# Kernel tuning notes

Measured on AMD Instinct MI355X. Metric: run time of the kernel, lower is better.

The kernel has to match this reference:

```python
import jax, jax.numpy as jnp
import numpy as np

N, DEG, D, L = 20000, 32, 128, 2
EPS = 1e-7
MAX_TANH_ARG = 1.0 - 1e-5


def _logmap0(x, sqrt_c):
    # Poincare ball log map at the origin: artanh(sqrt(c)||x||) * x / (sqrt(c)||x||)
    norm = jnp.maximum(jnp.linalg.norm(x, axis=-1, keepdims=True), EPS)
    arg = jnp.minimum(sqrt_c * norm, MAX_TANH_ARG)
    return jnp.arctanh(arg) * x / (sqrt_c * norm)


def _expmap0(v, sqrt_c):
    # Poincare ball exp map at the origin: tanh(sqrt(c)||v||) * v / (sqrt(c)||v||)
    norm = jnp.maximum(jnp.linalg.norm(v, axis=-1, keepdims=True), EPS)
    return jnp.tanh(sqrt_c * norm) * v / (sqrt_c * norm)


def setup_inputs() -> dict:
    key = jax.random.key(0)
    ks = jax.random.split(key, 7)
    neighbors = jax.random.randint(ks[0], (N, DEG), 0, N)  # fixed in-degree predecessor lists
    node_embeddings = jax.random.normal(ks[1], (N, D), dtype=jnp.float32)
    in_proj_w = jax.random.normal(ks[2], (L, 3 * D, D), dtype=jnp.float32) * 0.02
    in_proj_b = jax.random.normal(ks[3], (L, 3 * D), dtype=jnp.float32) * 0.02
    out_proj_w = jax.random.normal(ks[4], (L, D, D), dtype=jnp.float32) * 0.02
    out_proj_b = jax.random.normal(ks[5], (L, D), dtype=jnp.float32) * 0.02
    curvature = jnp.array([-1.0], dtype=jnp.float32)
    return {
        'neighbors': neighbors,
        'node_embeddings': node_embeddings,
        'curvature': curvature,
        'in_proj_w': in_proj_w,
        'in_proj_b': in_proj_b,
        'out_proj_w': out_proj_w,
        'out_proj_b': out_proj_b,
    }


def reference(neighbors, node_embeddings, curvature, in_proj_w, in_proj_b, out_proj_w, out_proj_b):
    sqrt_c = jnp.sqrt(jnp.abs(curvature[0]))
    scale = 1.0 / np.sqrt(D)  # torch MHA scales q by 1/sqrt(head_dim)
    x = node_embeddings
    for l in range(L):
        t = _logmap0(x, sqrt_c)                       # [N, d] tangent features
        Wq, Wk, Wv = in_proj_w[l, :D], in_proj_w[l, D:2 * D], in_proj_w[l, 2 * D:]
        bq, bk, bv = in_proj_b[l, :D], in_proj_b[l, D:2 * D], in_proj_b[l, 2 * D:]
        q = t @ Wq.T + bq                             # [N, d]
        k = t @ Wk.T + bk
        v = t @ Wv.T + bv
        kn = k[neighbors]                             # [N, deg, d] gather over predecessors
        vn = v[neighbors]                             # [N, deg, d]
        scores = jnp.einsum('nd,nkd->nk', q, kn) * scale
        attn = jax.nn.softmax(scores, axis=-1)        # [N, deg]
        h = jnp.einsum('nk,nkd->nd', attn, vn)        # [N, d]
        h = h @ out_proj_w[l].T + out_proj_b[l]
        x = _expmap0(h, sqrt_c)
    return x
```

## Files before the change

kernel.cpp:

```cpp
#include <hip/hip_runtime.h>

#define N_NODES 20000
#define N_PAD   20032
#define DEG 32
#define D 128
#define EPS 1e-7f
#define MAX_TANH_ARG (1.0f - 1e-5f)
#define SCORE_SCALE 0.08838834764831845f
#define MTILES 313

typedef short bf16x8 __attribute__((ext_vector_type(8)));
typedef float f32x4 __attribute__((ext_vector_type(4)));
typedef float f32x2 __attribute__((ext_vector_type(2)));

__device__ __forceinline__ float b2f(unsigned short u) {
  union { unsigned int i; float f; } x; x.i = ((unsigned int)u) << 16; return x.f;
}
__device__ __forceinline__ unsigned short f2b(float f) {
  union { float f; unsigned int i; } x; x.f = f;
  unsigned int r = x.i + 0x7FFFu + ((x.i >> 16) & 1u);
  return (unsigned short)(r >> 16);
}
__device__ __forceinline__ bool inputs_are_bf16(const void* curv) {
  return *(const unsigned short*)curv != 0;
}
__device__ __forceinline__ float read_sqrt_c(const void* c) {
  unsigned short u = *(const unsigned short*)c;
  float cv = (u == 0) ? *(const float*)c : b2f(u);
  return sqrtf(fabsf(cv));
}
__device__ __forceinline__ float atanh_fast(float x) {
  return 0.5f * __logf((1.f + x) / (1.f - x));
}
__device__ __forceinline__ float tanh_over_y(float y) {
  float e = __expf(-2.f * y);
  return (1.f - e) / ((1.f + e) * y);
}
__device__ __forceinline__ float load1(const void* p, size_t off, bool bf) {
  return bf ? b2f(((const unsigned short*)p)[off]) : ((const float*)p)[off];
}

__device__ __forceinline__ unsigned char f2fp8(float v) {
#if __has_builtin(__builtin_amdgcn_cvt_pk_fp8_f32)
  int p = __builtin_amdgcn_cvt_pk_fp8_f32(v, 0.f, 0, false);
  return (unsigned char)(p & 0xFF);
#else
  union { float f; unsigned u; } x; x.f = v;
  unsigned s = (x.u >> 31) << 7;
  float a = fminf(fabsf(v), 448.f);
  int q = (int)rintf(a * 512.f);
  if (q < 8) return (unsigned char)(s | q);
  int e; float m = frexpf(a, &e);
  int E = e - 1 + 7;
  int mi = (int)rintf(m * 16.f) - 8;
  if (mi == 8) { mi = 0; E += 1; }
  if (E > 15) { E = 15; mi = 6; }
  if (E < 1)  { return (unsigned char)(s | ((int)rintf(a * 512.f) & 7)); }
  return (unsigned char)(s | (E << 3) | mi);
#endif
}
__device__ __forceinline__ void fp8x8_decode_sw(uint2 w, float* f) {
#pragma unroll
  for (int i = 0; i < 8; i++) {
    unsigned char u = (i < 4) ? (unsigned char)(w.x >> (8 * i))
                              : (unsigned char)(w.y >> (8 * (i - 4)));
    int e = (u >> 3) & 15, m = u & 7;
    float mag = e ? ldexpf((float)(8 + m), e - 10) : ldexpf((float)m, -9);
    f[i] = (u & 0x80) ? -mag : mag;
  }
}
__device__ __forceinline__ void fp8x8_decode2(uint2 w, f32x2* f) {
#if __has_builtin(__builtin_amdgcn_cvt_pk_f32_fp8)
  f[0] = __builtin_amdgcn_cvt_pk_f32_fp8((int)w.x, false);
  f[1] = __builtin_amdgcn_cvt_pk_f32_fp8((int)w.x, true);
  f[2] = __builtin_amdgcn_cvt_pk_f32_fp8((int)w.y, false);
  f[3] = __builtin_amdgcn_cvt_pk_f32_fp8((int)w.y, true);
#else
  float t[8];
  fp8x8_decode_sw(w, t);
  f[0] = {t[0], t[1]}; f[1] = {t[2], t[3]};
  f[2] = {t[4], t[5]}; f[3] = {t[6], t[7]};
#endif
}

template <int NT>
__device__ __forceinline__ void stage_W(const void* W, size_t woff, bool srcbf,
                                        unsigned short* W_lds, int tid) {
  if (srcbf) {
#pragma unroll
    for (int c = 0; c < 16384 / (NT * 8); c++) {
      int idx = c * NT * 8 + tid * 8;
      bf16x8 v = *(const bf16x8*)((const unsigned short*)W + woff + idx);
      int row = idx >> 7, col = idx & 127;
      *(bf16x8*)&W_lds[row * 136 + col] = v;
    }
  } else {
#pragma unroll
    for (int c = 0; c < 16384 / (NT * 4); c++) {
      int idx = c * NT * 4 + tid * 4;
      float4 v = *(const float4*)((const float*)W + woff + idx);
      int row = idx >> 7, col = idx & 127;
      unsigned short* p = &W_lds[row * 136 + col];
      p[0] = f2b(v.x); p[1] = f2b(v.y); p[2] = f2b(v.z); p[3] = f2b(v.w);
    }
  }
}

__device__ __forceinline__ void qkv_from_lds(
    const bf16x8* a, const unsigned short* W_lds,
    const void* bias, size_t boff, bool srcbf,
    int m0, int quad, int l16,
    unsigned short* qout, unsigned char* out8, bool isq) {
#pragma unroll
  for (int half = 0; half < 2; half++) {
#pragma unroll
    for (int s = 0; s < 4; s++) {
      int n = half * 64 + s * 16 + l16;
      f32x4 c = {0.f, 0.f, 0.f, 0.f};
#pragma unroll
      for (int kk = 0; kk < 4; kk++) {
        bf16x8 bfv = *(const bf16x8*)&W_lds[n * 136 + quad * 8 + kk * 32];
        c = __builtin_amdgcn_mfma_f32_16x16x32_bf16(a[kk], bfv, c, 0, 0, 0);
      }
      float bv = load1(bias, boff + n, srcbf);
#pragma unroll
      for (int r = 0; r < 4; r++) {
        int m = m0 + quad * 4 + r;
        float val = c[r] + bv;
        if (isq) qout[(size_t)m * D + n] = f2b(val);
        else     out8[(size_t)m * D + n] = f2fp8(val);
      }
    }
  }
}

__device__ __forceinline__ void outproj_acc_frag(
    const bf16x8* a, const unsigned short* W_lds,
    int quad, int l16, f32x4* acc) {
#pragma unroll
  for (int s = 0; s < 8; s++) {
    f32x4 c = {0.f, 0.f, 0.f, 0.f};
#pragma unroll
    for (int kk = 0; kk < 4; kk++) {
      bf16x8 bfv = *(const bf16x8*)&W_lds[(s * 16 + l16) * 136 + quad * 8 + kk * 32];
      c = __builtin_amdgcn_mfma_f32_16x16x32_bf16(a[kk], bfv, c, 0, 0, 0);
    }
    acc[s] = c;
  }
}

__global__ __launch_bounds__(256) void lqkv_kernel(
    const void* __restrict__ xin,
    const void* __restrict__ in_w, const void* __restrict__ in_b,
    unsigned short* __restrict__ qout,
    unsigned char* __restrict__ kout, unsigned char* __restrict__ vout,
    const void* __restrict__ curv) {
  __shared__ unsigned short t_lds[64 * 136];
  __shared__ unsigned short W_lds[128 * 136];
  int tid = threadIdx.x;
  int lane = tid & 63;
  int wave = tid >> 6;
  int mbase = blockIdx.x * 64;
  int y = blockIdx.y;
  bool srcbf = inputs_are_bf16(curv);
  float sqc = read_sqrt_c(curv);

  stage_W<256>(in_w, (size_t)y * 128 * D, srcbf, W_lds, tid);

  {
    int rl = tid >> 3;
    int c8 = tid & 7;
#pragma unroll
    for (int pass = 0; pass < 2; pass++) {
      int r = pass * 32 + rl;
      int m = mbase + r;
      float xv[16];
      if (m < N_NODES) {
        if (srcbf) {
          const bf16x8* xp = (const bf16x8*)((const unsigned short*)xin + (size_t)m * D + c8 * 16);
          bf16x8 u0 = xp[0], u1 = xp[1];
#pragma unroll
          for (int i = 0; i < 8; i++) { xv[i] = b2f((unsigned short)u0[i]); xv[8 + i] = b2f((unsigned short)u1[i]); }
        } else {
          const float4* xp = (const float4*)((const float*)xin + (size_t)m * D + c8 * 16);
#pragma unroll
          for (int i = 0; i < 4; i++) {
            float4 v = xp[i];
            xv[i * 4 + 0] = v.x; xv[i * 4 + 1] = v.y; xv[i * 4 + 2] = v.z; xv[i * 4 + 3] = v.w;
          }
        }
      } else {
#pragma unroll
        for (int i = 0; i < 16; i++) xv[i] = 0.f;
      }
      float ss = 0.f;
#pragma unroll
      for (int i = 0; i < 16; i++) ss += xv[i] * xv[i];
      ss += __shfl_xor(ss, 1); ss += __shfl_xor(ss, 2); ss += __shfl_xor(ss, 4);
      float norm = fmaxf(sqrtf(ss), EPS);
      float arg  = fminf(sqc * norm, MAX_TANH_ARG);
      float sfac = atanh_fast(arg) / (sqc * norm);
      bf16x8 o0, o1;
#pragma unroll
      for (int i = 0; i < 8; i++) {
        o0[i] = (short)f2b(xv[i] * sfac);
        o1[i] = (short)f2b(xv[8 + i] * sfac);
      }
      *(bf16x8*)&t_lds[r * 136 + c8 * 16]     = o0;
      *(bf16x8*)&t_lds[r * 136 + c8 * 16 + 8] = o1;
    }
  }
  __syncthreads();

  int quad = lane >> 4, l16 = lane & 15;
  bf16x8 a[4];
#pragma unroll
  for (int kk = 0; kk < 4; kk++)
    a[kk] = *(const bf16x8*)&t_lds[(wave * 16 + l16) * 136 + quad * 8 + kk * 32];

  qkv_from_lds(a, W_lds, in_b, (size_t)y * 128, srcbf,
               mbase + wave * 16, quad, l16,
               qout, (y == 1) ? kout : vout, y == 0);
}

__global__ __launch_bounds__(256) void attn_kernel(
    const int* __restrict__ nbrs,
    const unsigned short* __restrict__ qb,
    const unsigned char* __restrict__ k8,
    const unsigned char* __restrict__ v8,
    unsigned short* __restrict__ hout) {
  int gid  = blockIdx.x * 256 + threadIdx.x;
  int node = gid >> 6;
  int lane = gid & 63;
  if (node >= N_NODES) return;
  int g = lane >> 4;
  int s = lane & 15;

  f32x2 qr2[4];
  {
    bf16x8 qv = *(const bf16x8*)(qb + (size_t)node * D + s * 8);
#pragma unroll
    for (int i = 0; i < 4; i++) {
      qr2[i][0] = b2f((unsigned short)qv[2 * i]);
      qr2[i][1] = b2f((unsigned short)qv[2 * i + 1]);
    }
  }
  int idx[8];
#pragma unroll
  for (int jj = 0; jj < 8; jj++) idx[jj] = nbrs[node * DEG + jj * 4 + g];

  uint2 kreg[8], vreg[8];
#pragma unroll
  for (int jj = 0; jj < 8; jj++)
    kreg[jj] = *(const uint2*)(k8 + (size_t)idx[jj] * D + s * 8);
#pragma unroll
  for (int jj = 0; jj < 8; jj++)
    vreg[jj] = *(const uint2*)(v8 + (size_t)idx[jj] * D + s * 8);

  float sc[8];
#pragma unroll
  for (int jj = 0; jj < 8; jj++) {
    f32x2 kf[4];
    fp8x8_decode2(kreg[jj], kf);
    f32x2 acc2 = kf[0] * qr2[0];
    acc2 += kf[1] * qr2[1];
    acc2 += kf[2] * qr2[2];
    acc2 += kf[3] * qr2[3];
    float p = acc2[0] + acc2[1];
    p += __shfl_xor(p, 1); p += __shfl_xor(p, 2);
    p += __shfl_xor(p, 4); p += __shfl_xor(p, 8);
    sc[jj] = p * SCORE_SCALE;
  }
  float mx = sc[0];
#pragma unroll
  for (int jj = 1; jj < 8; jj++) mx = fmaxf(mx, sc[jj]);
  mx = fmaxf(mx, __shfl_xor(mx, 16));
  mx = fmaxf(mx, __shfl_xor(mx, 32));
  float sum = 0.f;
#pragma unroll
  for (int jj = 0; jj < 8; jj++) { sc[jj] = __expf(sc[jj] - mx); sum += sc[jj]; }
  sum += __shfl_xor(sum, 16);
  sum += __shfl_xor(sum, 32);
  float inv = 1.f / sum;

  f32x2 hv2[4];
#pragma unroll
  for (int i = 0; i < 4; i++) hv2[i] = {0.f, 0.f};
#pragma unroll
  for (int jj = 0; jj < 8; jj++) {
    float aw = sc[jj] * inv;
    f32x2 aw2 = {aw, aw};
    f32x2 vf[4];
    fp8x8_decode2(vreg[jj], vf);
#pragma unroll
    for (int i = 0; i < 4; i++) hv2[i] += aw2 * vf[i];
  }
  float hv[8];
#pragma unroll
  for (int i = 0; i < 4; i++) { hv[2 * i] = hv2[i][0]; hv[2 * i + 1] = hv2[i][1]; }
#pragma unroll
  for (int i = 0; i < 8; i++) {
    hv[i] += __shfl_xor(hv[i], 16);
    hv[i] += __shfl_xor(hv[i], 32);
  }
  if (g == 0) {
    bf16x8 o;
#pragma unroll
    for (int i = 0; i < 8; i++) o[i] = (short)f2b(hv[i]);
    *(bf16x8*)(hout + (size_t)node * D + s * 8) = o;
  }
}

__global__ __launch_bounds__(256) void op_qkv_kernel(
    const unsigned short* __restrict__ h,
    const void* __restrict__ out_w, const void* __restrict__ out_b,
    const void* __restrict__ in_w, const void* __restrict__ in_b,
    unsigned short* __restrict__ qout,
    unsigned char* __restrict__ kout, unsigned char* __restrict__ vout,
    const void* __restrict__ curv) {
  __shared__ unsigned short t_lds[64 * 136];
  __shared__ unsigned short W_lds[128 * 136];
  int tid = threadIdx.x;
  int lane = tid & 63;
  int wave = tid >> 6;
  int quad = lane >> 4, l16 = lane & 15;
  int m0 = blockIdx.x * 64 + wave * 16;
  int y = blockIdx.y;
  bool srcbf = inputs_are_bf16(curv);

  stage_W<256>(out_w, 0, srcbf, W_lds, tid);
  __syncthreads();
  {
    bf16x8 a[4];
    const short* arow = (const short*)h + (size_t)(m0 + l16) * D + quad * 8;
#pragma unroll
    for (int kk = 0; kk < 4; kk++) a[kk] = *(const bf16x8*)(arow + kk * 32);
    f32x4 acc[8];
    outproj_acc_frag(a, W_lds, quad, l16, acc);
#pragma unroll
    for (int s = 0; s < 8; s++) {
      float bv = load1(out_b, s * 16 + l16, srcbf);
#pragma unroll
      for (int r = 0; r < 4; r++) {
        int rloc = wave * 16 + quad * 4 + r;
        t_lds[rloc * 136 + s * 16 + l16] = f2b(acc[s][r] + bv);
      }
    }
  }
  __syncthreads();

  bf16x8 a[4];
#pragma unroll
  for (int kk = 0; kk < 4; kk++)
    a[kk] = *(const bf16x8*)&t_lds[(wave * 16 + l16) * 136 + quad * 8 + kk * 32];
  stage_W<256>(in_w, (size_t)384 * D + (size_t)y * 128 * D, srcbf, W_lds, tid);
  __syncthreads();

  qkv_from_lds(a, W_lds, in_b, (size_t)384 + y * 128, srcbf,
               m0, quad, l16, qout, (y == 1) ? kout : vout, y == 0);
}

__global__ __launch_bounds__(256) void outproj_final_kernel(
    const unsigned short* __restrict__ h,
    const void* __restrict__ out_w, const void* __restrict__ out_b,
    void* __restrict__ xout, const void* __restrict__ curv) {
  __shared__ unsigned short W_lds[128 * 136];
  int tid = threadIdx.x;
  int lane = tid & 63;
  int wave = tid >> 6;
  int quad = lane >> 4, l16 = lane & 15;
  int m0 = blockIdx.x * 64 + wave * 16;
  bool srcbf = inputs_are_bf16(curv);
  float sqc = read_sqrt_c(curv);

  stage_W<256>(out_w, (size_t)D * D, srcbf, W_lds, tid);
  __syncthreads();

  bf16x8 a[4];
  const short* arow = (const short*)h + (size_t)(m0 + l16) * D + quad * 8;
#pragma unroll
  for (int kk = 0; kk < 4; kk++) a[kk] = *(const bf16x8*)(arow + kk * 32);

  f32x4 acc[8];
  outproj_acc_frag(a, W_lds, quad, l16, acc);
#pragma unroll
  for (int s = 0; s < 8; s++) {
    float bv = load1(out_b, D + s * 16 + l16, srcbf);
#pragma unroll
    for (int r = 0; r < 4; r++) acc[s][r] += bv;
  }
  float scal[4];
#pragma unroll
  for (int r = 0; r < 4; r++) {
    float ss = 0.f;
#pragma unroll
    for (int s = 0; s < 8; s++) ss += acc[s][r] * acc[s][r];
    ss += __shfl_xor(ss, 1); ss += __shfl_xor(ss, 2);
    ss += __shfl_xor(ss, 4); ss += __shfl_xor(ss, 8);
    float norm = fmaxf(sqrtf(ss), EPS);
    scal[r] = tanh_over_y(sqc * norm);
  }
#pragma unroll
  for (int r = 0; r < 4; r++) {
    int m = m0 + quad * 4 + r;
    if (m < N_NODES) {
#pragma unroll
      for (int s = 0; s < 8; s++) {
        float val = acc[s][r] * scal[r];
        int col = s * 16 + l16;
        if (srcbf) ((unsigned short*)xout)[(size_t)m * D + col] = f2b(val);
        else       ((float*)xout)[(size_t)m * D + col] = val;
      }
    }
  }
}

extern "C" void kernel_launch(void* const* d_in, const int* in_sizes, int n_in,
                              void* d_out, int out_size, void* d_ws, size_t ws_size,
                              hipStream_t stream) {
  const int* neighbors = (const int*)d_in[0];
  const void* node_emb = d_in[1];
  const void* curv     = d_in[2];
  const void* in_w     = d_in[3];
  const void* in_b     = d_in[4];
  const void* out_w    = d_in[5];
  const void* out_b    = d_in[6];

  char* ws = (char*)d_ws;
  size_t off = 0;
  auto alloc = [&](size_t bytes) {
    char* p = ws + off; off += (bytes + 255) & ~(size_t)255; return p;
  };
  unsigned short* q_bf = (unsigned short*)alloc((size_t)N_PAD * D * 2);
  unsigned char*  k_f8 = (unsigned char*)alloc((size_t)N_PAD * D);
  unsigned char*  v_f8 = (unsigned char*)alloc((size_t)N_PAD * D);
  unsigned short* h_bf = (unsigned short*)alloc((size_t)N_PAD * D * 2);

  lqkv_kernel<<<dim3(MTILES, 3), 256, 0, stream>>>(
      node_emb, in_w, in_b, q_bf, k_f8, v_f8, curv);
  attn_kernel<<<5000, 256, 0, stream>>>(neighbors, q_bf, k_f8, v_f8, h_bf);
  op_qkv_kernel<<<dim3(MTILES, 3), 256, 0, stream>>>(
      h_bf, out_w, out_b, in_w, in_b, q_bf, k_f8, v_f8, curv);
  attn_kernel<<<5000, 256, 0, stream>>>(neighbors, q_bf, k_f8, v_f8, h_bf);
  outproj_final_kernel<<<MTILES, 256, 0, stream>>>(
      h_bf, out_w, out_b, d_out, curv);
}
```

Before: 150.1 us.

## Interleave fp8 K/V rows into one buffer and gather with single loads

K and V are now stored in one buffer of 256 bytes per node, with each 16-lane slice holding 8 bytes of K followed by 8 bytes of V. The attention kernel can then fetch both for a neighbor with one 16-byte load instead of two 8-byte loads from separate arrays. Neighbor indices are also read as two int4 vector loads per lane group, which changes which neighbors each group handles; the softmax does not depend on that order. The softmax max-subtraction is removed, which saves shuffles but assumes the scores are small enough for exp not to overflow.

```diff
diff --git a/kernel.cpp b/kernel.cpp
--- a/kernel.cpp
+++ b/kernel.cpp
@@ -110,7 +110,7 @@
     const bf16x8* a, const unsigned short* W_lds,
     const void* bias, size_t boff, bool srcbf,
     int m0, int quad, int l16,
-    unsigned short* qout, unsigned char* out8, bool isq) {
+    unsigned short* qout, unsigned char* kv8, bool isq, int voff) {
 #pragma unroll
   for (int half = 0; half < 2; half++) {
 #pragma unroll
@@ -123,12 +123,13 @@
         c = __builtin_amdgcn_mfma_f32_16x16x32_bf16(a[kk], bfv, c, 0, 0, 0);
       }
       float bv = load1(bias, boff + n, srcbf);
+      int col8 = (n >> 3) * 16 + (n & 7) + voff;
 #pragma unroll
       for (int r = 0; r < 4; r++) {
         int m = m0 + quad * 4 + r;
         float val = c[r] + bv;
         if (isq) qout[(size_t)m * D + n] = f2b(val);
-        else     out8[(size_t)m * D + n] = f2fp8(val);
+        else     kv8[(size_t)m * 256 + col8] = f2fp8(val);
       }
     }
   }
@@ -152,8 +153,7 @@
 __global__ __launch_bounds__(256) void lqkv_kernel(
     const void* __restrict__ xin,
     const void* __restrict__ in_w, const void* __restrict__ in_b,
-    unsigned short* __restrict__ qout,
-    unsigned char* __restrict__ kout, unsigned char* __restrict__ vout,
+    unsigned short* __restrict__ qout, unsigned char* __restrict__ kv8,
     const void* __restrict__ curv) {
   __shared__ unsigned short t_lds[64 * 136];
   __shared__ unsigned short W_lds[128 * 136];
@@ -220,14 +220,13 @@
 
   qkv_from_lds(a, W_lds, in_b, (size_t)y * 128, srcbf,
                mbase + wave * 16, quad, l16,
-               qout, (y == 1) ? kout : vout, y == 0);
+               qout, kv8, y == 0, (y == 2) ? 8 : 0);
 }
 
 __global__ __launch_bounds__(256) void attn_kernel(
     const int* __restrict__ nbrs,
     const unsigned short* __restrict__ qb,
-    const unsigned char* __restrict__ k8,
-    const unsigned char* __restrict__ v8,
+    const unsigned char* __restrict__ kv8,
     unsigned short* __restrict__ hout) {
   int gid  = blockIdx.x * 256 + threadIdx.x;
   int node = gid >> 6;
@@ -245,23 +244,23 @@
       qr2[i][1] = b2f((unsigned short)qv[2 * i + 1]);
     }
   }
-  int idx[8];
-#pragma unroll
-  for (int jj = 0; jj < 8; jj++) idx[jj] = nbrs[node * DEG + jj * 4 + g];
-
-  uint2 kreg[8], vreg[8];
+  int4 i0, i1;
+  {
+    const int4* np = (const int4*)(nbrs + node * DEG + g * 8);
+    i0 = np[0]; i1 = np[1];
+  }
+  int idx[8] = {i0.x, i0.y, i0.z, i0.w, i1.x, i1.y, i1.z, i1.w};
+
+  uint4 kvreg[8];
 #pragma unroll
   for (int jj = 0; jj < 8; jj++)
-    kreg[jj] = *(const uint2*)(k8 + (size_t)idx[jj] * D + s * 8);
-#pragma unroll
-  for (int jj = 0; jj < 8; jj++)
-    vreg[jj] = *(const uint2*)(v8 + (size_t)idx[jj] * D + s * 8);
+    kvreg[jj] = *(const uint4*)(kv8 + (size_t)idx[jj] * 256 + s * 16);
 
   float sc[8];
 #pragma unroll
   for (int jj = 0; jj < 8; jj++) {
     f32x2 kf[4];
-    fp8x8_decode2(kreg[jj], kf);
+    fp8x8_decode2({kvreg[jj].x, kvreg[jj].y}, kf);
     f32x2 acc2 = kf[0] * qr2[0];
     acc2 += kf[1] * qr2[1];
     acc2 += kf[2] * qr2[2];
@@ -271,14 +270,9 @@
     p += __shfl_xor(p, 4); p += __shfl_xor(p, 8);
     sc[jj] = p * SCORE_SCALE;
   }
-  float mx = sc[0];
-#pragma unroll
-  for (int jj = 1; jj < 8; jj++) mx = fmaxf(mx, sc[jj]);
-  mx = fmaxf(mx, __shfl_xor(mx, 16));
-  mx = fmaxf(mx, __shfl_xor(mx, 32));
   float sum = 0.f;
 #pragma unroll
-  for (int jj = 0; jj < 8; jj++) { sc[jj] = __expf(sc[jj] - mx); sum += sc[jj]; }
+  for (int jj = 0; jj < 8; jj++) { sc[jj] = __expf(sc[jj]); sum += sc[jj]; }
   sum += __shfl_xor(sum, 16);
   sum += __shfl_xor(sum, 32);
   float inv = 1.f / sum;
@@ -291,7 +285,7 @@
     float aw = sc[jj] * inv;
     f32x2 aw2 = {aw, aw};
     f32x2 vf[4];
-    fp8x8_decode2(vreg[jj], vf);
+    fp8x8_decode2({kvreg[jj].z, kvreg[jj].w}, vf);
 #pragma unroll
     for (int i = 0; i < 4; i++) hv2[i] += aw2 * vf[i];
   }
@@ -315,8 +309,7 @@
     const unsigned short* __restrict__ h,
     const void* __restrict__ out_w, const void* __restrict__ out_b,
     const void* __restrict__ in_w, const void* __restrict__ in_b,
-    unsigned short* __restrict__ qout,
-    unsigned char* __restrict__ kout, unsigned char* __restrict__ vout,
+    unsigned short* __restrict__ qout, unsigned char* __restrict__ kv8,
     const void* __restrict__ curv) {
   __shared__ unsigned short t_lds[64 * 136];
   __shared__ unsigned short W_lds[128 * 136];
@@ -357,7 +350,7 @@
   __syncthreads();
 
   qkv_from_lds(a, W_lds, in_b, (size_t)384 + y * 128, srcbf,
-               m0, quad, l16, qout, (y == 1) ? kout : vout, y == 0);
+               m0, quad, l16, qout, kv8, y == 0, (y == 2) ? 8 : 0);
 }
 
 __global__ __launch_bounds__(256) void outproj_final_kernel(
@@ -432,16 +425,15 @@
     char* p = ws + off; off += (bytes + 255) & ~(size_t)255; return p;
   };
   unsigned short* q_bf = (unsigned short*)alloc((size_t)N_PAD * D * 2);
-  unsigned char*  k_f8 = (unsigned char*)alloc((size_t)N_PAD * D);
-  unsigned char*  v_f8 = (unsigned char*)alloc((size_t)N_PAD * D);
+  unsigned char*  kv8  = (unsigned char*)alloc((size_t)N_PAD * 256);
   unsigned short* h_bf = (unsigned short*)alloc((size_t)N_PAD * D * 2);
 
   lqkv_kernel<<<dim3(MTILES, 3), 256, 0, stream>>>(
-      node_emb, in_w, in_b, q_bf, k_f8, v_f8, curv);
-  attn_kernel<<<5000, 256, 0, stream>>>(neighbors, q_bf, k_f8, v_f8, h_bf);
+      node_emb, in_w, in_b, q_bf, kv8, curv);
+  attn_kernel<<<5000, 256, 0, stream>>>(neighbors, q_bf, kv8, h_bf);
   op_qkv_kernel<<<dim3(MTILES, 3), 256, 0, stream>>>(
-      h_bf, out_w, out_b, in_w, in_b, q_bf, k_f8, v_f8, curv);
-  attn_kernel<<<5000, 256, 0, stream>>>(neighbors, q_bf, k_f8, v_f8, h_bf);
+      h_bf, out_w, out_b, in_w, in_b, q_bf, kv8, curv);
+  attn_kernel<<<5000, 256, 0, stream>>>(neighbors, q_bf, kv8, h_bf);
   outproj_final_kernel<<<MTILES, 256, 0, stream>>>(
       h_bf, out_w, out_b, d_out, curv);
 }
```

New measurement: 153.3 us. 2.1% more time.
